# Kernel optimization log

Measured on AMD Instinct MI355X. Metric: run time of the kernel, lower is better.

The kernel has to match this reference:

```python
import jax, jax.numpy as jnp
import numpy as np

HIDDEN, NH, HD, EPS = 1024, 16, 64, 1e-6


def _phi(x):
    # Positive feature map (elu + 1), standard for linear attention memory.
    return jax.nn.elu(x) + 1.0


def setup_inputs() -> dict:
    key = jax.random.key(0)
    ks = jax.random.split(key, 10)
    sc = 1.0 / np.sqrt(HIDDEN)  # keep activations sane
    return {
        "hidden_states": jax.random.normal(ks[0], (4, 8192, HIDDEN), jnp.float32),
        "Wq": jax.random.normal(ks[1], (HIDDEN, HIDDEN), jnp.float32) * sc,
        "bq": jax.random.normal(ks[2], (HIDDEN,), jnp.float32) * 0.01,
        "Wk": jax.random.normal(ks[3], (HIDDEN, HIDDEN), jnp.float32) * sc,
        "bk": jax.random.normal(ks[4], (HIDDEN,), jnp.float32) * 0.01,
        "Wv": jax.random.normal(ks[5], (HIDDEN, HIDDEN), jnp.float32) * sc,
        "bv": jax.random.normal(ks[6], (HIDDEN,), jnp.float32) * 0.01,
        "Wo": jax.random.normal(ks[7], (HIDDEN, HIDDEN), jnp.float32) * sc,
        "S0": jax.random.normal(ks[8], (4, NH, HD, HD), jnp.float32),
        "z0": jax.random.uniform(ks[9], (4, NH, HD), jnp.float32) + 0.1,
    }


def reference(hidden_states, Wq, bq, Wk, bk, Wv, bv, Wo, S0, z0):
    B, S, _ = hidden_states.shape
    # Q/K/V projections (nn.Linear: x @ W.T + b), split heads -> [B, H, S, D]
    def heads(x):
        return x.reshape(B, S, NH, HD).transpose(0, 2, 1, 3)

    q = heads(hidden_states @ Wq.T + bq)
    k = heads(hidden_states @ Wk.T + bk)
    v = heads(hidden_states @ Wv.T + bv)

    qf = _phi(q)
    kf = _phi(k)

    # RETRIEVE from memory state (pre-update, as in the torch forward):
    # num[b,h,s,e] = sum_d qf[b,h,s,d] * S0[b,h,d,e]; den = qf . z0 + eps
    num = jnp.einsum("bhsd,bhde->bhse", qf, S0)
    den = jnp.einsum("bhsd,bhd->bhs", qf, z0) + EPS
    out = num / den[..., None]                       # [B, H, S, D]

    # UPDATE memory (new state; mutation side-effect in torch):
    S_new = S0 + jnp.einsum("bhsd,bhse->bhde", kf, v)
    z_new = z0 + kf.sum(axis=2)
    del S_new, z_new  # state update computed for fidelity; output is result only

    # Merge heads and output projection (no bias)
    out = out.transpose(0, 2, 1, 3).reshape(B, S, NH * HD)
    return out @ Wo.T
```

## Files before the change

kernel.cpp:

```cpp
#include <hip/hip_runtime.h>
#include <hip/hip_bf16.h>


#define EPS 1e-6f

typedef __attribute__((ext_vector_type(8))) short short8;
typedef __attribute__((ext_vector_type(4))) float f32x4;

typedef __attribute__((address_space(3))) void lds_t;
typedef const __attribute__((address_space(1))) void gbl_t;

__device__ __forceinline__ unsigned short f2bf(float f) {
    unsigned int u = __float_as_uint(f);
    u += 0x7fffu + ((u >> 16) & 1u);
    return (unsigned short)(u >> 16);
}

__global__ void cvt_bf16_kernel(const float* __restrict__ in,
                                unsigned short* __restrict__ out, int n8) {
    for (int i = blockIdx.x * blockDim.x + threadIdx.x; i < n8;
         i += gridDim.x * blockDim.x) {
        float4 a = reinterpret_cast<const float4*>(in)[2 * i];
        float4 b = reinterpret_cast<const float4*>(in)[2 * i + 1];
        short8 v;
        v[0] = (short)f2bf(a.x); v[1] = (short)f2bf(a.y);
        v[2] = (short)f2bf(a.z); v[3] = (short)f2bf(a.w);
        v[4] = (short)f2bf(b.x); v[5] = (short)f2bf(b.y);
        v[6] = (short)f2bf(b.z); v[7] = (short)f2bf(b.w);
        reinterpret_cast<short8*>(out)[i] = v;
    }
}

template <int EPI>
__global__ void gemm_bt_kernel(const unsigned short* __restrict__ A,
                               const unsigned short* __restrict__ Bw,
                               const float* __restrict__ bias,
                               void* __restrict__ Cp,
                               int M, int N, int K) {
    __shared__ unsigned short Alds[128][32];
    __shared__ unsigned short Blds[128][32];
    const int tid = threadIdx.x;
    const int wave = tid >> 6, lane = tid & 63;
    const int wm = wave >> 1, wn = wave & 1;
    const int tm = blockIdx.y * 128, tn = blockIdx.x * 128;

    const int srow = lane >> 2;
    const int scol = (lane & 3) * 8;

    f32x4 acc[4][4] = {};

    for (int k0 = 0; k0 < K; k0 += 32) {
#pragma unroll
        for (int i = 0; i < 2; ++i) {
            const unsigned short* ga =
                A + (size_t)(tm + i * 64 + wave * 16 + srow) * K + (k0 + scol);
            __builtin_amdgcn_global_load_lds((gbl_t*)ga,
                (lds_t*)&Alds[i * 64 + wave * 16][0], 16, 0, 0);
            const unsigned short* gb =
                Bw + (size_t)(tn + i * 64 + wave * 16 + srow) * K + (k0 + scol);
            __builtin_amdgcn_global_load_lds((gbl_t*)gb,
                (lds_t*)&Blds[i * 64 + wave * 16][0], 16, 0, 0);
        }
        __syncthreads();

        short8 af[4], bfr[4];
#pragma unroll
        for (int mi = 0; mi < 4; ++mi)
            af[mi] = *reinterpret_cast<const short8*>(
                &Alds[wm * 64 + mi * 16 + (lane & 15)][(lane >> 4) * 8]);
#pragma unroll
        for (int ni = 0; ni < 4; ++ni)
            bfr[ni] = *reinterpret_cast<const short8*>(
                &Blds[wn * 64 + ni * 16 + (lane & 15)][(lane >> 4) * 8]);
#pragma unroll
        for (int mi = 0; mi < 4; ++mi)
#pragma unroll
            for (int ni = 0; ni < 4; ++ni)
                acc[mi][ni] = __builtin_amdgcn_mfma_f32_16x16x32_bf16(
                    af[mi], bfr[ni], acc[mi][ni], 0, 0, 0);
        __syncthreads();
    }

#pragma unroll
    for (int mi = 0; mi < 4; ++mi)
#pragma unroll
        for (int ni = 0; ni < 4; ++ni)
#pragma unroll
            for (int j = 0; j < 4; ++j) {
                int r = tm + wm * 64 + mi * 16 + (lane >> 4) * 4 + j;
                int c = tn + wn * 64 + ni * 16 + (lane & 15);
                float v = acc[mi][ni][j];
                if (EPI == 0) {
                    v += bias[c];
                    v = v > 0.f ? v + 1.f : __expf(v);
                    ((unsigned short*)Cp)[(size_t)r * N + c] = f2bf(v);
                } else {
                    ((float*)Cp)[(size_t)r * N + c] = v;
                }
            }
}

__global__ void retrieve_kernel(const unsigned short* __restrict__ qf,
                                const float* __restrict__ S0,
                                const float* __restrict__ z0,
                                unsigned short* __restrict__ mid) {
    __shared__ unsigned short Bt[64][72];
    const int tid = threadIdx.x;
    const int wave = tid >> 6, lane = tid & 63;
    const int bh = blockIdx.y;
    const int b = bh >> 4, h = bh & 15;

    const float* S = S0 + (size_t)bh * 4096;
#pragma unroll
    for (int it = 0; it < 16; ++it) {
        int idx = it * 256 + tid;
        int d = idx >> 6, e = idx & 63;
        Bt[e][d] = f2bf(S[idx]);
    }
    const float* z = z0 + bh * 64;
    short8 zf[2];
#pragma unroll
    for (int ks = 0; ks < 2; ++ks)
#pragma unroll
        for (int i = 0; i < 8; ++i)
            zf[ks][i] = (short)f2bf(z[ks * 32 + (lane >> 4) * 8 + i]);
    __syncthreads();

    const int srow0 = blockIdx.x * 256 + wave * 64;
    f32x4 num[4][4] = {};
    f32x4 den[4] = {};
#pragma unroll
    for (int ks = 0; ks < 2; ++ks) {
        short8 af[4];
#pragma unroll
        for (int mi = 0; mi < 4; ++mi) {
            size_t row = (size_t)b * 8192 + srow0 + mi * 16 + (lane & 15);
            af[mi] = *reinterpret_cast<const short8*>(
                &qf[row * 1024 + h * 64 + ks * 32 + (lane >> 4) * 8]);
        }
#pragma unroll
        for (int mi = 0; mi < 4; ++mi) {
#pragma unroll
            for (int ni = 0; ni < 4; ++ni) {
                short8 bfr = *reinterpret_cast<const short8*>(
                    &Bt[ni * 16 + (lane & 15)][ks * 32 + (lane >> 4) * 8]);
                num[mi][ni] = __builtin_amdgcn_mfma_f32_16x16x32_bf16(
                    af[mi], bfr, num[mi][ni], 0, 0, 0);
            }
            den[mi] = __builtin_amdgcn_mfma_f32_16x16x32_bf16(
                af[mi], zf[ks], den[mi], 0, 0, 0);
        }
    }
#pragma unroll
    for (int mi = 0; mi < 4; ++mi)
#pragma unroll
        for (int ni = 0; ni < 4; ++ni)
#pragma unroll
            for (int j = 0; j < 4; ++j) {
                size_t row = (size_t)b * 8192 + srow0 + mi * 16 + (lane >> 4) * 4 + j;
                int c = h * 64 + ni * 16 + (lane & 15);
                float v = num[mi][ni][j] / (den[mi][j] + EPS);
                mid[row * 1024 + c] = f2bf(v);
            }
}

extern "C" void kernel_launch(void* const* d_in, const int* in_sizes, int n_in,
                              void* d_out, int out_size, void* d_ws, size_t ws_size,
                              hipStream_t stream) {
    const float* X  = (const float*)d_in[0];
    const float* Wq = (const float*)d_in[1];
    const float* bq = (const float*)d_in[2];
    const float* Wo = (const float*)d_in[7];
    const float* S0 = (const float*)d_in[8];
    const float* z0 = (const float*)d_in[9];
    float* out = (float*)d_out;

    char* ws = (char*)d_ws;
    unsigned short* Xb  = (unsigned short*)ws;
    unsigned short* qf  = (unsigned short*)(ws + 67108864);
    unsigned short* Wqb = (unsigned short*)(ws + 134217728);
    unsigned short* Wob = (unsigned short*)(ws + 136314880);

    cvt_bf16_kernel<<<2048, 256, 0, stream>>>(X,  Xb,  33554432 / 8);
    cvt_bf16_kernel<<<512,  256, 0, stream>>>(Wq, Wqb, 1048576 / 8);
    cvt_bf16_kernel<<<512,  256, 0, stream>>>(Wo, Wob, 1048576 / 8);

    dim3 g(8, 256);
    gemm_bt_kernel<0><<<g, 256, 0, stream>>>(Xb, Wqb, bq, qf, 32768, 1024, 1024);
    retrieve_kernel<<<dim3(32, 64), 256, 0, stream>>>(qf, S0, z0, Xb );
    gemm_bt_kernel<1><<<g, 256, 0, stream>>>(Xb, Wob, nullptr, out, 32768, 1024, 1024);
}
```

Before: 471.9 us.

## Fuse retrieval into Q-projection GEMM, double-buffer LDS, swizzle blocks, merge weight casts

After: 428.6 us. -9.2%, faster.

```diff
diff --git a/kernel.cpp b/kernel.cpp
--- a/kernel.cpp
+++ b/kernel.cpp
@@ -31,47 +31,106 @@
     }
 }
 
-template <int EPI>
-__global__ void gemm_bt_kernel(const unsigned short* __restrict__ A,
-                               const unsigned short* __restrict__ Bw,
-                               const float* __restrict__ bias,
-                               void* __restrict__ Cp,
-                               int M, int N, int K) {
-    __shared__ unsigned short Alds[128][32];
-    __shared__ unsigned short Blds[128][32];
+__global__ void cvt_w_kernel(const float* __restrict__ w0,
+                             const float* __restrict__ w1,
+                             unsigned short* __restrict__ o0,
+                             unsigned short* __restrict__ o1, int n8) {
+    int i = blockIdx.x * blockDim.x + threadIdx.x;
+    const float* in = (i < n8) ? w0 : w1;
+    unsigned short* out = (i < n8) ? o0 : o1;
+    int j = (i < n8) ? i : i - n8;
+    float4 a = reinterpret_cast<const float4*>(in)[2 * j];
+    float4 b = reinterpret_cast<const float4*>(in)[2 * j + 1];
+    short8 v;
+    v[0] = (short)f2bf(a.x); v[1] = (short)f2bf(a.y);
+    v[2] = (short)f2bf(a.z); v[3] = (short)f2bf(a.w);
+    v[4] = (short)f2bf(b.x); v[5] = (short)f2bf(b.y);
+    v[6] = (short)f2bf(b.z); v[7] = (short)f2bf(b.w);
+    reinterpret_cast<short8*>(out)[j] = v;
+}
+
+#define STAGE(AL, BL, buf, k0)                                                   \
+    {                                                                            \
+        _Pragma("unroll")                                                        \
+        for (int i_ = 0; i_ < 2; ++i_) {                                         \
+            const unsigned short* ga_ =                                          \
+                A + (size_t)(tm + i_ * 64 + wave * 16 + srow) * 1024 + ((k0) + scol); \
+            __builtin_amdgcn_global_load_lds((gbl_t*)ga_,                        \
+                (lds_t*)&AL[buf][i_ * 64 + wave * 16][0], 16, 0, 0);             \
+            const unsigned short* gb_ =                                          \
+                Bw + (size_t)(tn + i_ * 64 + wave * 16 + srow) * 1024 + ((k0) + scol); \
+            __builtin_amdgcn_global_load_lds((gbl_t*)gb_,                        \
+                (lds_t*)&BL[buf][i_ * 64 + wave * 16][0], 16, 0, 0);             \
+        }                                                                        \
+    }
+
+__global__ __launch_bounds__(256, 3)
+void gemm_qs_kernel(const unsigned short* __restrict__ A,
+                    const unsigned short* __restrict__ Bw,
+                    const float* __restrict__ bias,
+                    const float* __restrict__ S0,
+                    const float* __restrict__ z0,
+                    unsigned short* __restrict__ mid) {
+    __shared__ union {
+        struct {
+            unsigned short Alds[2][128][32];
+            unsigned short Blds[2][128][32];
+        } s;
+        unsigned short Q[128][136];
+    } u;
+    __shared__ unsigned short S0t[2][64][72];
+
     const int tid = threadIdx.x;
     const int wave = tid >> 6, lane = tid & 63;
     const int wm = wave >> 1, wn = wave & 1;
-    const int tm = blockIdx.y * 128, tn = blockIdx.x * 128;
+
+    const int bid = blockIdx.y * gridDim.x + blockIdx.x;
+    const int swz = (bid & 7) * 256 + (bid >> 3);
+    const int bx = swz & 7, by = swz >> 3;
+    const int tm = by * 128, tn = bx * 128;
+    const int b = by >> 6;
+    const int h0 = bx * 2;
 
     const int srow = lane >> 2;
     const int scol = (lane & 3) * 8;
 
+#pragma unroll
+    for (int hh = 0; hh < 2; ++hh) {
+        const float* S = S0 + (size_t)(b * 16 + h0 + hh) * 4096;
+#pragma unroll
+        for (int it = 0; it < 16; ++it) {
+            int idx = it * 256 + tid;
+            S0t[hh][idx & 63][idx >> 6] = f2bf(S[idx]);
+        }
+    }
+    const float* z = z0 + (b * 16 + h0 + wn) * 64;
+    short8 zf[2];
+#pragma unroll
+    for (int ks = 0; ks < 2; ++ks)
+#pragma unroll
+        for (int i = 0; i < 8; ++i)
+            zf[ks][i] = (short)f2bf(z[ks * 32 + (lane >> 4) * 8 + i]);
+    float bv[4];
+#pragma unroll
+    for (int ni = 0; ni < 4; ++ni)
+        bv[ni] = bias[tn + wn * 64 + ni * 16 + (lane & 15)];
+
     f32x4 acc[4][4] = {};
-
-    for (int k0 = 0; k0 < K; k0 += 32) {
-#pragma unroll
-        for (int i = 0; i < 2; ++i) {
-            const unsigned short* ga =
-                A + (size_t)(tm + i * 64 + wave * 16 + srow) * K + (k0 + scol);
-            __builtin_amdgcn_global_load_lds((gbl_t*)ga,
-                (lds_t*)&Alds[i * 64 + wave * 16][0], 16, 0, 0);
-            const unsigned short* gb =
-                Bw + (size_t)(tn + i * 64 + wave * 16 + srow) * K + (k0 + scol);
-            __builtin_amdgcn_global_load_lds((gbl_t*)gb,
-                (lds_t*)&Blds[i * 64 + wave * 16][0], 16, 0, 0);
-        }
-        __syncthreads();
-
+    STAGE(u.s.Alds, u.s.Blds, 0, 0);
+    __syncthreads();
+
+    for (int t = 0; t < 32; ++t) {
+        if (t < 31) STAGE(u.s.Alds, u.s.Blds, (t + 1) & 1, (t + 1) * 32);
+        const int buf = t & 1;
         short8 af[4], bfr[4];
 #pragma unroll
         for (int mi = 0; mi < 4; ++mi)
             af[mi] = *reinterpret_cast<const short8*>(
-                &Alds[wm * 64 + mi * 16 + (lane & 15)][(lane >> 4) * 8]);
+                &u.s.Alds[buf][wm * 64 + mi * 16 + (lane & 15)][(lane >> 4) * 8]);
 #pragma unroll
         for (int ni = 0; ni < 4; ++ni)
             bfr[ni] = *reinterpret_cast<const short8*>(
-                &Blds[wn * 64 + ni * 16 + (lane & 15)][(lane >> 4) * 8]);
+                &u.s.Blds[buf][wn * 64 + ni * 16 + (lane & 15)][(lane >> 4) * 8]);
 #pragma unroll
         for (int mi = 0; mi < 4; ++mi)
 #pragma unroll
@@ -84,83 +143,103 @@
 #pragma unroll
     for (int mi = 0; mi < 4; ++mi)
 #pragma unroll
-        for (int ni = 0; ni < 4; ++ni)
+        for (int ni = 0; ni < 4; ++ni) {
+            const int lc = wn * 64 + ni * 16 + (lane & 15);
 #pragma unroll
             for (int j = 0; j < 4; ++j) {
-                int r = tm + wm * 64 + mi * 16 + (lane >> 4) * 4 + j;
-                int c = tn + wn * 64 + ni * 16 + (lane & 15);
-                float v = acc[mi][ni][j];
-                if (EPI == 0) {
-                    v += bias[c];
-                    v = v > 0.f ? v + 1.f : __expf(v);
-                    ((unsigned short*)Cp)[(size_t)r * N + c] = f2bf(v);
-                } else {
-                    ((float*)Cp)[(size_t)r * N + c] = v;
-                }
-            }
-}
-
-__global__ void retrieve_kernel(const unsigned short* __restrict__ qf,
-                                const float* __restrict__ S0,
-                                const float* __restrict__ z0,
-                                unsigned short* __restrict__ mid) {
-    __shared__ unsigned short Bt[64][72];
+                const int lr = wm * 64 + mi * 16 + (lane >> 4) * 4 + j;
+                float v = acc[mi][ni][j] + bv[ni];
+                v = v > 0.f ? v + 1.f : __expf(v);
+                u.Q[lr][lc] = f2bf(v);
+            }
+        }
+    __syncthreads();
+
+    f32x4 o2[4][4] = {};
+    f32x4 d2[4] = {};
+#pragma unroll
+    for (int ks = 0; ks < 2; ++ks) {
+        short8 af2[4];
+#pragma unroll
+        for (int mi = 0; mi < 4; ++mi)
+            af2[mi] = *reinterpret_cast<const short8*>(
+                &u.Q[wm * 64 + mi * 16 + (lane & 15)][wn * 64 + ks * 32 + (lane >> 4) * 8]);
+#pragma unroll
+        for (int mi = 0; mi < 4; ++mi) {
+#pragma unroll
+            for (int ni = 0; ni < 4; ++ni) {
+                short8 b2 = *reinterpret_cast<const short8*>(
+                    &S0t[wn][ni * 16 + (lane & 15)][ks * 32 + (lane >> 4) * 8]);
+                o2[mi][ni] = __builtin_amdgcn_mfma_f32_16x16x32_bf16(
+                    af2[mi], b2, o2[mi][ni], 0, 0, 0);
+            }
+            d2[mi] = __builtin_amdgcn_mfma_f32_16x16x32_bf16(
+                af2[mi], zf[ks], d2[mi], 0, 0, 0);
+        }
+    }
+#pragma unroll
+    for (int mi = 0; mi < 4; ++mi)
+#pragma unroll
+        for (int ni = 0; ni < 4; ++ni)
+#pragma unroll
+            for (int j = 0; j < 4; ++j) {
+                size_t gr = (size_t)tm + wm * 64 + mi * 16 + (lane >> 4) * 4 + j;
+                int gc = tn + wn * 64 + ni * 16 + (lane & 15);
+                mid[gr * 1024 + gc] = f2bf(o2[mi][ni][j] / (d2[mi][j] + EPS));
+            }
+}
+
+__global__ void gemm_o_kernel(const unsigned short* __restrict__ A,
+                              const unsigned short* __restrict__ Bw,
+                              float* __restrict__ out) {
+    __shared__ unsigned short Alds[2][128][32];
+    __shared__ unsigned short Blds[2][128][32];
     const int tid = threadIdx.x;
     const int wave = tid >> 6, lane = tid & 63;
-    const int bh = blockIdx.y;
-    const int b = bh >> 4, h = bh & 15;
-
-    const float* S = S0 + (size_t)bh * 4096;
-#pragma unroll
-    for (int it = 0; it < 16; ++it) {
-        int idx = it * 256 + tid;
-        int d = idx >> 6, e = idx & 63;
-        Bt[e][d] = f2bf(S[idx]);
-    }
-    const float* z = z0 + bh * 64;
-    short8 zf[2];
-#pragma unroll
-    for (int ks = 0; ks < 2; ++ks)
-#pragma unroll
-        for (int i = 0; i < 8; ++i)
-            zf[ks][i] = (short)f2bf(z[ks * 32 + (lane >> 4) * 8 + i]);
+    const int wm = wave >> 1, wn = wave & 1;
+
+    const int bid = blockIdx.y * gridDim.x + blockIdx.x;
+    const int swz = (bid & 7) * 256 + (bid >> 3);
+    const int bx = swz & 7, by = swz >> 3;
+    const int tm = by * 128, tn = bx * 128;
+
+    const int srow = lane >> 2;
+    const int scol = (lane & 3) * 8;
+
+    f32x4 acc[4][4] = {};
+    STAGE(Alds, Blds, 0, 0);
     __syncthreads();
 
-    const int srow0 = blockIdx.x * 256 + wave * 64;
-    f32x4 num[4][4] = {};
-    f32x4 den[4] = {};
-#pragma unroll
-    for (int ks = 0; ks < 2; ++ks) {
-        short8 af[4];
-#pragma unroll
-        for (int mi = 0; mi < 4; ++mi) {
-            size_t row = (size_t)b * 8192 + srow0 + mi * 16 + (lane & 15);
+    for (int t = 0; t < 32; ++t) {
+        if (t < 31) STAGE(Alds, Blds, (t + 1) & 1, (t + 1) * 32);
+        const int buf = t & 1;
+        short8 af[4], bfr[4];
+#pragma unroll
+        for (int mi = 0; mi < 4; ++mi)
             af[mi] = *reinterpret_cast<const short8*>(
-                &qf[row * 1024 + h * 64 + ks * 32 + (lane >> 4) * 8]);
-        }
-#pragma unroll
-        for (int mi = 0; mi < 4; ++mi) {
-#pragma unroll
-            for (int ni = 0; ni < 4; ++ni) {
-                short8 bfr = *reinterpret_cast<const short8*>(
-                    &Bt[ni * 16 + (lane & 15)][ks * 32 + (lane >> 4) * 8]);
-                num[mi][ni] = __builtin_amdgcn_mfma_f32_16x16x32_bf16(
-                    af[mi], bfr, num[mi][ni], 0, 0, 0);
-            }
-            den[mi] = __builtin_amdgcn_mfma_f32_16x16x32_bf16(
-                af[mi], zf[ks], den[mi], 0, 0, 0);
-        }
-    }
+                &Alds[buf][wm * 64 + mi * 16 + (lane & 15)][(lane >> 4) * 8]);
+#pragma unroll
+        for (int ni = 0; ni < 4; ++ni)
+            bfr[ni] = *reinterpret_cast<const short8*>(
+                &Blds[buf][wn * 64 + ni * 16 + (lane & 15)][(lane >> 4) * 8]);
+#pragma unroll
+        for (int mi = 0; mi < 4; ++mi)
+#pragma unroll
+            for (int ni = 0; ni < 4; ++ni)
+                acc[mi][ni] = __builtin_amdgcn_mfma_f32_16x16x32_bf16(
+                    af[mi], bfr[ni], acc[mi][ni], 0, 0, 0);
+        __syncthreads();
+    }
+
 #pragma unroll
     for (int mi = 0; mi < 4; ++mi)
 #pragma unroll
         for (int ni = 0; ni < 4; ++ni)
 #pragma unroll
             for (int j = 0; j < 4; ++j) {
-                size_t row = (size_t)b * 8192 + srow0 + mi * 16 + (lane >> 4) * 4 + j;
-                int c = h * 64 + ni * 16 + (lane & 15);
-                float v = num[mi][ni][j] / (den[mi][j] + EPS);
-                mid[row * 1024 + c] = f2bf(v);
+                size_t gr = (size_t)tm + wm * 64 + mi * 16 + (lane >> 4) * 4 + j;
+                int gc = tn + wn * 64 + ni * 16 + (lane & 15);
+                out[gr * 1024 + gc] = acc[mi][ni][j];
             }
 }
 
@@ -177,16 +256,14 @@
 
     char* ws = (char*)d_ws;
     unsigned short* Xb  = (unsigned short*)ws;
-    unsigned short* qf  = (unsigned short*)(ws + 67108864);
+    unsigned short* mid = (unsigned short*)(ws + 67108864);
     unsigned short* Wqb = (unsigned short*)(ws + 134217728);
     unsigned short* Wob = (unsigned short*)(ws + 136314880);
 
-    cvt_bf16_kernel<<<2048, 256, 0, stream>>>(X,  Xb,  33554432 / 8);
-    cvt_bf16_kernel<<<512,  256, 0, stream>>>(Wq, Wqb, 1048576 / 8);
-    cvt_bf16_kernel<<<512,  256, 0, stream>>>(Wo, Wob, 1048576 / 8);
+    cvt_bf16_kernel<<<2048, 256, 0, stream>>>(X, Xb, 33554432 / 8);
+    cvt_w_kernel<<<1024, 256, 0, stream>>>(Wq, Wo, Wqb, Wob, 1048576 / 8);
 
     dim3 g(8, 256);
-    gemm_bt_kernel<0><<<g, 256, 0, stream>>>(Xb, Wqb, bq, qf, 32768, 1024, 1024);
-    retrieve_kernel<<<dim3(32, 64), 256, 0, stream>>>(qf, S0, z0, Xb );
-    gemm_bt_kernel<1><<<g, 256, 0, stream>>>(Xb, Wob, nullptr, out, 32768, 1024, 1024);
-}
+    gemm_qs_kernel<<<g, 256, 0, stream>>>(Xb, Wqb, bq, S0, z0, mid);
+    gemm_o_kernel<<<g, 256, 0, stream>>>(mid, Wob, out);
+}
```
